# Kernel tuning notes

Measured on AMD Instinct MI355X. Metric: run time of the kernel, lower is better.

Reference implementation:

```python
import jax, jax.numpy as jnp
import numpy as np

N, G, H = 262144, 512, 16
EPS = 1e-5

Q_MAT = jnp.array([[0.0, 0.0, 1.0], [1.0, 0.0, 0.0], [0.0, 1.0, 0.0]], dtype=jnp.float32)
Q_TENSOR = jnp.kron(Q_MAT, Q_MAT)  # 9x9


def setup_inputs() -> dict:
    key = jax.random.key(0)
    ks = jax.random.split(key, 10)
    # sorted node->graph ids, every graph guaranteed non-empty
    gid = jnp.sort(jnp.concatenate([
        jnp.arange(G, dtype=jnp.int32),
        jax.random.randint(ks[0], (N - G,), 0, G, dtype=jnp.int32)]))
    return {
        'x00': jax.random.normal(ks[1], (N, 4 * H), jnp.float32),
        'x10': jax.random.normal(ks[2], (N, H, 3), jnp.float32),
        'x01': jax.random.normal(ks[3], (N, H, 3), jnp.float32),
        'x11': jax.random.normal(ks[4], (N, H, 9), jnp.float32),
        'pos': jax.random.normal(ks[5], (N, 6), jnp.float32),
        'graph_ids': gid,
        'num_graphs': G,
        'bn_gamma': jnp.ones((4 * H,), jnp.float32),
        'bn_beta': jnp.zeros((4 * H,), jnp.float32),
        'lin_w': jax.random.normal(ks[6], (3, 4 * H), jnp.float32) * 0.1,
        'lin_b': jnp.zeros((3,), jnp.float32),
        'w10': jax.random.normal(ks[7], (1, H), jnp.float32) * 0.3,
        'w01': jax.random.normal(ks[8], (1, H), jnp.float32) * 0.3,
        'w11': jax.random.normal(ks[9], (1, H), jnp.float32) * 0.3,
    }


def _graph_norm(x, seg, num_seg, gamma, beta):
    # per-graph mean/var normalization over nodes ('gn')
    cnt = jax.ops.segment_sum(jnp.ones((x.shape[0],), x.dtype), seg, num_segments=num_seg)
    cnt = jnp.maximum(cnt, 1.0)[:, None]
    mean = jax.ops.segment_sum(x, seg, num_segments=num_seg) / cnt
    var = jax.ops.segment_sum(x * x, seg, num_segments=num_seg) / cnt - mean * mean
    xn = (x - mean[seg]) * jax.lax.rsqrt(var[seg] + EPS)
    return xn * gamma + beta


def _segment_softmax(logits, seg, num_seg):
    m = jax.ops.segment_max(logits, seg, num_segments=num_seg)
    e = jnp.exp(logits - m[seg])
    s = jax.ops.segment_sum(e, seg, num_segments=num_seg)
    return e / s[seg]


def _project_r(r_vector):
    # SVD projection to nearest rotation (sign-corrected)
    norm = jnp.clip(jnp.linalg.norm(r_vector, axis=1, keepdims=True), 1e-5, None)
    r_vector = r_vector / jax.lax.stop_gradient(norm)  # norm is detached in torch
    # einops 'b (d c) -> b c d' with c=3
    r_ = jnp.transpose(r_vector.reshape(-1, 3, 3), (0, 2, 1))
    U, S, Vh = jnp.linalg.svd(r_, full_matrices=False)
    rot_pos = U @ Vh
    Vh_neg = Vh.at[:, 2, :].multiply(-1.0)
    rot_neg = U @ Vh_neg
    det = jnp.linalg.det(rot_pos)
    return jnp.where(det[:, None, None] > 0, rot_pos, rot_neg)


def reference(x00, x10, x01, x11, pos, graph_ids, num_graphs,
              bn_gamma, bn_beta, lin_w, lin_b, w10, w01, w11):
    seg = graph_ids
    Gn = num_graphs
    # BN('gn') + Linear -> 3 per-node logits
    xn = _graph_norm(x00, seg, Gn, bn_gamma, bn_beta)
    logits = xn @ lin_w.T + lin_b                       # [N,3]
    W = _segment_softmax(logits, seg, Gn)                # per-graph softmax over nodes
    w0, w1, w2 = W[:, 0:1], W[:, 1:2], W[:, 2:3]
    # weighted per-graph sums (dgl.sum_nodes)
    ab = jnp.concatenate([x10, x01], axis=-1)            # [N,H,6]
    mean_ab = jax.ops.segment_sum(ab * w1[:, :, None], seg, num_segments=Gn)   # [G,H,6]
    r_sum = jax.ops.segment_sum(x11 * w0[:, :, None], seg, num_segments=Gn)    # [G,H,9]
    m1m2 = jax.ops.segment_sum(pos * w2, seg, num_segments=Gn)                 # [G,6]
    m1, m2 = m1m2[:, 0:3], m1m2[:, 3:]
    # GLinear head: channel-mixing H -> 1 per degree type (no bias)
    out10 = jnp.einsum('oc,gcd->god', w10, mean_ab[:, :, :3])[:, 0, :]  # [G,3]
    out01 = jnp.einsum('oc,gcd->god', w01, mean_ab[:, :, 3:6])[:, 0, :]
    out11 = jnp.einsum('oc,gcd->god', w11, r_sum)[:, 0, :]              # [G,9]
    # permutation back to input frame
    r_vector = jnp.einsum('ij,gj->gi', Q_TENSOR, out11)
    trans_b = jnp.einsum('ij,gj->gi', Q_MAT, out01)
    trans_a = jnp.einsum('ij,gj->gi', Q_MAT, out10)
    rot_mat = _project_r(r_vector)
    t = m2 + trans_b - (rot_mat @ m1[..., None])[..., 0] - (rot_mat @ trans_a[..., None])[..., 0]
    return rot_mat, t, r_vector
```

## Files before the change

kernel.cpp:

```cpp
#include <hip/hip_runtime.h>
#include <cstdint>
#include <cstddef>

#define GG 512
#define NF 64
#define EPSF 1e-5f

__device__ __forceinline__ void atomAddF(float* p, float v) {
    unsafeAtomicAdd(p, v);
}

__global__ __launch_bounds__(256) void k_stats(const float* __restrict__ x00, const int* __restrict__ gid,
                        float* __restrict__ gsum, float* __restrict__ gsq,
                        float* __restrict__ gcnt, int N)
{
    int w = (blockIdx.x * blockDim.x + threadIdx.x) >> 6;
    int lane = threadIdx.x & 63;
    long base = (long)w * 64;
    int gf = gid[base];
    int gl = gid[base + 63];
    if (gf == gl) {
        const float4* p = reinterpret_cast<const float4*>(x00 + base * NF) + lane;
        float s0=0,s1=0,s2=0,s3=0,q0=0,q1=0,q2=0,q3=0;
        #pragma unroll
        for (int k = 0; k < 16; ++k) {
            float4 v = p[k * 64];
            s0+=v.x; s1+=v.y; s2+=v.z; s3+=v.w;
            q0=fmaf(v.x,v.x,q0); q1=fmaf(v.y,v.y,q1); q2=fmaf(v.z,v.z,q2); q3=fmaf(v.w,v.w,q3);
        }
        #pragma unroll
        for (int m = 16; m < 64; m <<= 1) {
            s0+=__shfl_xor(s0,m); s1+=__shfl_xor(s1,m); s2+=__shfl_xor(s2,m); s3+=__shfl_xor(s3,m);
            q0+=__shfl_xor(q0,m); q1+=__shfl_xor(q1,m); q2+=__shfl_xor(q2,m); q3+=__shfl_xor(q3,m);
        }
        if (lane < 16) {
            float* ds = gsum + gf * NF + lane * 4;
            float* dq = gsq  + gf * NF + lane * 4;
            atomAddF(ds+0,s0); atomAddF(ds+1,s1); atomAddF(ds+2,s2); atomAddF(ds+3,s3);
            atomAddF(dq+0,q0); atomAddF(dq+1,q1); atomAddF(dq+2,q2); atomAddF(dq+3,q3);
        }
        if (lane == 0) atomAddF(&gcnt[gf], 64.0f);
    } else {
        int myg = gid[base + lane];
        int cur = gf;
        float s = 0.f, q = 0.f, cnt = 0.f;
        for (int k = 0; k < 64; ++k) {
            int g = __shfl(myg, k);
            if (g != cur) {
                atomAddF(&gsum[cur * NF + lane], s);
                atomAddF(&gsq [cur * NF + lane], q);
                if (lane == 0) atomAddF(&gcnt[cur], cnt);
                s = q = cnt = 0.f; cur = g;
            }
            float v = x00[(base + k) * NF + lane];
            s += v; q = fmaf(v, v, q); cnt += 1.f;
        }
        atomAddF(&gsum[cur * NF + lane], s);
        atomAddF(&gsq [cur * NF + lane], q);
        if (lane == 0) atomAddF(&gcnt[cur], cnt);
    }
}

__global__ void k_prep(const float* __restrict__ gsum, const float* __restrict__ gsq,
                       const float* __restrict__ gcnt,
                       const float* __restrict__ gamma, const float* __restrict__ beta,
                       const float* __restrict__ lin_w, const float* __restrict__ lin_b,
                       float* __restrict__ Aeff, float* __restrict__ Beff)
{
    int g = blockIdx.x;
    int c = threadIdx.x;
    float cnt = fmaxf(gcnt[g], 1.f);
    float mean = gsum[g * NF + c] / cnt;
    float var  = gsq [g * NF + c] / cnt - mean * mean;
    float rs = rsqrtf(var + EPSF);
    float ga = gamma[c], be = beta[c];
    #pragma unroll
    for (int j = 0; j < 3; ++j) {
        float wv = lin_w[j * NF + c];
        Aeff[((long)g * 3 + j) * NF + c] = rs * ga * wv;
        float term = (be - mean * rs * ga) * wv;
        #pragma unroll
        for (int m = 32; m; m >>= 1) term += __shfl_xor(term, m);
        if (c == 0) Beff[g * 3 + j] = term + lin_b[j];
    }
}

__global__ __launch_bounds__(128) void k_logits(const float* __restrict__ x00, const int* __restrict__ gid,
                         const float* __restrict__ pos,
                         const float* __restrict__ Aeff, const float* __restrict__ Beff,
                         float* __restrict__ ebp, float* __restrict__ accum, int N)
{
    __shared__ float T2[2][64 * 68];
    int wid = threadIdx.x >> 6;
    int lane = threadIdx.x & 63;
    long chunk = (long)blockIdx.x * 2 + wid;
    long base = chunk * 64;
    float* T = T2[wid];

    const float* src = x00 + base * NF;
    #pragma unroll
    for (int k = 0; k < 16; ++k) {
        int fl = k * 256 + lane * 4;
        float4 v = *reinterpret_cast<const float4*>(src + fl);
        int n = fl >> 6, c = fl & 63;
        *reinterpret_cast<float4*>(&T[n * 68 + c]) = v;
    }
    __syncthreads();

    int gf = gid[base], gl = gid[base + 63];
    float l0, l1, l2;
    int g_l;
    if (gf == gl) {
        g_l = gf;
        const float* ap = Aeff + (size_t)gf * 192;
        float a0a=0,a0b=0,a1a=0,a1b=0,a2a=0,a2b=0;
        #pragma unroll
        for (int t = 0; t < 16; ++t) {
            float4 xv = *reinterpret_cast<const float4*>(&T[lane * 68 + 4 * t]);
            float4 w0 = *reinterpret_cast<const float4*>(ap + 4 * t);
            float4 w1 = *reinterpret_cast<const float4*>(ap + 64 + 4 * t);
            float4 w2 = *reinterpret_cast<const float4*>(ap + 128 + 4 * t);
            a0a = fmaf(xv.x,w0.x,fmaf(xv.y,w0.y,a0a)); a0b = fmaf(xv.z,w0.z,fmaf(xv.w,w0.w,a0b));
            a1a = fmaf(xv.x,w1.x,fmaf(xv.y,w1.y,a1a)); a1b = fmaf(xv.z,w1.z,fmaf(xv.w,w1.w,a1b));
            a2a = fmaf(xv.x,w2.x,fmaf(xv.y,w2.y,a2a)); a2b = fmaf(xv.z,w2.z,fmaf(xv.w,w2.w,a2b));
        }
        l0 = a0a + a0b + Beff[gf*3+0];
        l1 = a1a + a1b + Beff[gf*3+1];
        l2 = a2a + a2b + Beff[gf*3+2];
    } else {
        g_l = gid[base + lane];
        const float* ap = Aeff + (size_t)g_l * 192;
        float a0=0,a1=0,a2=0;
        #pragma unroll
        for (int t = 0; t < 16; ++t) {
            float4 xv = *reinterpret_cast<const float4*>(&T[lane * 68 + 4 * t]);
            float4 w0 = *reinterpret_cast<const float4*>(ap + 4 * t);
            float4 w1 = *reinterpret_cast<const float4*>(ap + 64 + 4 * t);
            float4 w2 = *reinterpret_cast<const float4*>(ap + 128 + 4 * t);
            a0 = fmaf(xv.x,w0.x,fmaf(xv.y,w0.y,fmaf(xv.z,w0.z,fmaf(xv.w,w0.w,a0))));
            a1 = fmaf(xv.x,w1.x,fmaf(xv.y,w1.y,fmaf(xv.z,w1.z,fmaf(xv.w,w1.w,a1))));
            a2 = fmaf(xv.x,w2.x,fmaf(xv.y,w2.y,fmaf(xv.z,w2.z,fmaf(xv.w,w2.w,a2))));
        }
        l0 = a0 + Beff[g_l*3+0];
        l1 = a1 + Beff[g_l*3+1];
        l2 = a2 + Beff[g_l*3+2];
    }
    float e0 = expf(l0), e1 = expf(l1), e2 = expf(l2);
    long node = base + lane;
    ebp[node]            = e0;
    ebp[(long)N + node]  = e1;
    ebp[2L * N + node]   = e2;

    const float* pp = pos + node * 6;
    float2 v01 = *reinterpret_cast<const float2*>(pp);
    float2 v23 = *reinterpret_cast<const float2*>(pp + 2);
    float2 v45 = *reinterpret_cast<const float2*>(pp + 4);
    float p0 = v01.x*e2, p1 = v01.y*e2, p2 = v23.x*e2, p3 = v23.y*e2, p4 = v45.x*e2, p5 = v45.y*e2;
    if (gf == gl) {
        #pragma unroll
        for (int m = 1; m < 64; m <<= 1) {
            e0+=__shfl_xor(e0,m); e1+=__shfl_xor(e1,m); e2+=__shfl_xor(e2,m);
            p0+=__shfl_xor(p0,m); p1+=__shfl_xor(p1,m); p2+=__shfl_xor(p2,m);
            p3+=__shfl_xor(p3,m); p4+=__shfl_xor(p4,m); p5+=__shfl_xor(p5,m);
        }
        if (lane == 0) {
            float* dst = accum + (long)gf * 32;
            atomAddF(dst+16,p0); atomAddF(dst+17,p1); atomAddF(dst+18,p2);
            atomAddF(dst+19,p3); atomAddF(dst+20,p4); atomAddF(dst+21,p5);
            atomAddF(dst+22,e0); atomAddF(dst+23,e1); atomAddF(dst+24,e2);
        }
    } else {
        float* dst = accum + (long)g_l * 32;
        atomAddF(dst+16,p0); atomAddF(dst+17,p1); atomAddF(dst+18,p2);
        atomAddF(dst+19,p3); atomAddF(dst+20,p4); atomAddF(dst+21,p5);
        atomAddF(dst+22,e0); atomAddF(dst+23,e1); atomAddF(dst+24,e2);
    }
}

__global__ __launch_bounds__(256) void k_wsum(const float* __restrict__ x10, const float* __restrict__ x01,
                       const float* __restrict__ x11,
                       const float* __restrict__ ebp, const int* __restrict__ gid,
                       const float* __restrict__ w10, const float* __restrict__ w01,
                       const float* __restrict__ w11,
                       float* __restrict__ accum, int N)
{
    __shared__ float Tb[4][240];
    int wid = threadIdx.x >> 6;
    int w = (blockIdx.x * blockDim.x + threadIdx.x) >> 6;
    int lane = threadIdx.x & 63;
    long base = (long)w * 64;
    float* T = Tb[wid];

    const float* p; long stride; const float* eb; int accOff; bool wr = true;
    float wt0, wt1, wt2, wt3;
    if (lane < 12) {
        p = x10 + lane * 4; stride = 48; eb = ebp + N; accOff = lane * 4;
        int f = lane * 4;
        wt0 = w10[f/3]; wt1 = w10[(f+1)/3]; wt2 = w10[(f+2)/3]; wt3 = w10[(f+3)/3];
    } else if (lane < 24) {
        p = x01 + (lane - 12) * 4; stride = 48; eb = ebp + N; accOff = 48 + (lane - 12) * 4;
        int f = (lane - 12) * 4;
        wt0 = w01[f/3]; wt1 = w01[(f+1)/3]; wt2 = w01[(f+2)/3]; wt3 = w01[(f+3)/3];
    } else if (lane < 60) {
        p = x11 + (lane - 24) * 4; stride = 144; eb = ebp; accOff = 96 + (lane - 24) * 4;
        int f = (lane - 24) * 4;
        wt0 = w11[f/9]; wt1 = w11[(f+1)/9]; wt2 = w11[(f+2)/9]; wt3 = w11[(f+3)/9];
    } else {
        p = x11 + 140; stride = 144; eb = ebp; accOff = 0; wr = false;
        wt0 = wt1 = wt2 = wt3 = 0.f;
    }

    float a0=0,a1=0,a2=0,a3=0;
    const float* pp = p + base * stride;
    const float* ep = eb + base;

    auto flush = [&](int g) {
        asm volatile("" ::: "memory");
        if (wr) {
            T[accOff+0] = a0*wt0; T[accOff+1] = a1*wt1;
            T[accOff+2] = a2*wt2; T[accOff+3] = a3*wt3;
        }
        asm volatile("s_waitcnt lgkmcnt(0)" ::: "memory");
        if (lane < 15) {
            int off, strd;
            if (lane < 3)      { off = lane;            strd = 3; }
            else if (lane < 6) { off = 48 + (lane - 3); strd = 3; }
            else               { off = 96 + (lane - 6); strd = 9; }
            float s = 0.f;
            #pragma unroll
            for (int c = 0; c < 16; ++c) s += T[off + c * strd];
            atomAddF(accum + (long)g * 32 + lane, s);
        }
        asm volatile("s_waitcnt lgkmcnt(0)" ::: "memory");
    };

    int gf = gid[base], gl = gid[base + 63];
    if (gf == gl) {
        #pragma unroll 8
        for (int k = 0; k < 64; ++k) {
            float e = ep[k];
            float4 v = *reinterpret_cast<const float4*>(pp + (long)k * stride);
            a0 = fmaf(v.x,e,a0); a1 = fmaf(v.y,e,a1); a2 = fmaf(v.z,e,a2); a3 = fmaf(v.w,e,a3);
        }
        flush(gf);
    } else {
        int myg = gid[base + lane];
        int cur = gf;
        for (int k = 0; k < 64; ++k) {
            int g = __shfl(myg, k);
            if (g != cur) { flush(cur); a0=a1=a2=a3=0.f; cur = g; }
            float e = ep[k];
            float4 v = *reinterpret_cast<const float4*>(pp + (long)k * stride);
            a0 = fmaf(v.x,e,a0); a1 = fmaf(v.y,e,a1); a2 = fmaf(v.z,e,a2); a3 = fmaf(v.w,e,a3);
        }
        flush(cur);
    }
}

#define JROT(p, q) do { \
    float apq_ = S[p][q]; \
    if (fabsf(apq_) > 1e-20f) { \
        float app_ = S[p][p], aqq_ = S[q][q]; \
        float tau_ = (aqq_ - app_) / (2.0f * apq_); \
        float tt_ = copysignf(1.0f, tau_) / (fabsf(tau_) + sqrtf(1.0f + tau_ * tau_)); \
        float cc_ = 1.0f / sqrtf(1.0f + tt_ * tt_); \
        float ssn_ = tt_ * cc_; \
        _Pragma("unroll") for (int kk = 0; kk < 3; ++kk) { \
            float skp = S[kk][p], skq = S[kk][q]; \
            S[kk][p] = cc_ * skp - ssn_ * skq; S[kk][q] = ssn_ * skp + cc_ * skq; } \
        _Pragma("unroll") for (int kk = 0; kk < 3; ++kk) { \
            float spk = S[p][kk], sqk = S[q][kk]; \
            S[p][kk] = cc_ * spk - ssn_ * sqk; S[q][kk] = ssn_ * spk + cc_ * sqk; } \
        _Pragma("unroll") for (int kk = 0; kk < 3; ++kk) { \
            float vkp = V[kk][p], vkq = V[kk][q]; \
            V[kk][p] = cc_ * vkp - ssn_ * vkq; V[kk][q] = ssn_ * vkp + cc_ * vkq; } \
    } \
} while (0)

__global__ void k_final(const float* __restrict__ accum, float* __restrict__ out)
{
    int g = blockIdx.x * blockDim.x + threadIdx.x;
    if (g >= GG) return;
    const float* A_ = accum + (long)g * 32;
    float i0 = 1.f / A_[22], i1 = 1.f / A_[23], i2 = 1.f / A_[24];

    float o10[3], o01[3], o11[9];
    #pragma unroll
    for (int d = 0; d < 3; ++d) { o10[d] = A_[d] * i1; o01[d] = A_[3 + d] * i1; }
    #pragma unroll
    for (int d = 0; d < 9; ++d) o11[d] = A_[6 + d] * i0;

    float m1v[3], m2v[3];
    #pragma unroll
    for (int d = 0; d < 3; ++d) { m1v[d] = A_[16 + d] * i2; m2v[d] = A_[19 + d] * i2; }

    int sig[3]; sig[0] = 2; sig[1] = 0; sig[2] = 1;
    float rv[9];
    #pragma unroll
    for (int a = 0; a < 3; ++a)
        #pragma unroll
        for (int b = 0; b < 3; ++b)
            rv[a * 3 + b] = o11[sig[a] * 3 + sig[b]];
    float ta[3], tb[3];
    #pragma unroll
    for (int a = 0; a < 3; ++a) { ta[a] = o10[sig[a]]; tb[a] = o01[sig[a]]; }

    float nn = 0.f;
    #pragma unroll
// ... 56 lines not shown
    R[0][2] = u0x * e0z + u1x * e1z + u2x * c2z;
    R[1][0] = u0y * e0x + u1y * e1x + u2y * c2x;
    R[1][1] = u0y * e0y + u1y * e1y + u2y * c2y;
    R[1][2] = u0y * e0z + u1y * e1z + u2y * c2z;
    R[2][0] = u0z * e0x + u1z * e1x + u2z * c2x;
    R[2][1] = u0z * e0y + u1z * e1y + u2z * c2y;
    R[2][2] = u0z * e0z + u1z * e1z + u2z * c2z;

    float tv[3];
    #pragma unroll
    for (int a = 0; a < 3; ++a) {
        float acc = m2v[a] + tb[a];
        #pragma unroll
        for (int b = 0; b < 3; ++b) acc -= R[a][b] * (m1v[b] + ta[b]);
        tv[a] = acc;
    }

    #pragma unroll
    for (int k = 0; k < 9; ++k) out[(long)g * 9 + k] = R[k / 3][k % 3];
    #pragma unroll
    for (int a = 0; a < 3; ++a) out[(long)GG * 9 + (long)g * 3 + a] = tv[a];
    #pragma unroll
    for (int k = 0; k < 9; ++k) out[(long)GG * 12 + (long)g * 9 + k] = rv[k];
}

extern "C" void kernel_launch(void* const* d_in, const int* in_sizes, int n_in,
                              void* d_out, int out_size, void* d_ws, size_t ws_size,
                              hipStream_t stream)
{
    const float* x00   = (const float*)d_in[0];
    const float* x10   = (const float*)d_in[1];
    const float* x01   = (const float*)d_in[2];
    const float* x11   = (const float*)d_in[3];
    const float* pos   = (const float*)d_in[4];
    const int*   gid   = (const int*)d_in[5];
    const float* gamma = (const float*)d_in[7];
    const float* beta  = (const float*)d_in[8];
    const float* lin_w = (const float*)d_in[9];
    const float* lin_b = (const float*)d_in[10];
    const float* w10   = (const float*)d_in[11];
    const float* w01   = (const float*)d_in[12];
    const float* w11   = (const float*)d_in[13];
    float* out = (float*)d_out;

    const int N = in_sizes[0] / NF;

    float* ws = (float*)d_ws;
    float* gsum  = ws;
    float* gsq   = gsum + GG * 64;
    float* gcnt  = gsq + GG * 64;
    float* accum = gcnt + GG;
    float* Aeff  = accum + GG * 32;
    float* Beff  = Aeff + GG * 192;
    float* ebp   = Beff + GG * 3;

    size_t zeroBytes = (size_t)(GG * 64 * 2 + GG + GG * 32) * sizeof(float);
    hipMemsetAsync(d_ws, 0, zeroBytes, stream);

    int nwave64 = N / 64;
    int blocks64 = nwave64 / 4;
    int blocksLg = (N / 64) / 2;

    k_stats <<<blocks64, 256, 0, stream>>>(x00, gid, gsum, gsq, gcnt, N);
    k_prep  <<<GG, 64, 0, stream>>>(gsum, gsq, gcnt, gamma, beta, lin_w, lin_b, Aeff, Beff);
    k_logits<<<blocksLg, 128, 0, stream>>>(x00, gid, pos, Aeff, Beff, ebp, accum, N);
    k_wsum  <<<blocks64, 256, 0, stream>>>(x10, x01, x11, ebp, gid, w10, w01, w11, accum, N);
    k_final <<<(GG + 63) / 64, 64, 0, stream>>>(accum, out);
}
```

Before: 187.5 us.

## Split weighted-sum kernel into LDS-staged x11 and x10/x01 kernels

Replaces the single wave-per-64-nodes weighted-sum kernel, which had strided per-lane float4 loads, with two block-per-64-nodes kernels. Each block loads its tile coalesced into shared memory and applies the H-channel mixing per node before the segment reduction. Uniform-graph tiles are reduced through shared memory with one atomic per output. Mixed tiles instead issue per-element atomics, which adds an extra kernel launch and more shared-memory traffic and occupancy pressure (about 37KB LDS per block for x11).

```diff
diff --git a/kernel.cpp b/kernel.cpp
--- a/kernel.cpp
+++ b/kernel.cpp
@@ -177,83 +177,142 @@
     }
 }
 
-__global__ __launch_bounds__(256) void k_wsum(const float* __restrict__ x10, const float* __restrict__ x01,
-                       const float* __restrict__ x11,
-                       const float* __restrict__ ebp, const int* __restrict__ gid,
-                       const float* __restrict__ w10, const float* __restrict__ w01,
-                       const float* __restrict__ w11,
-                       float* __restrict__ accum, int N)
-{
-    __shared__ float Tb[4][240];
-    int wid = threadIdx.x >> 6;
-    int w = (blockIdx.x * blockDim.x + threadIdx.x) >> 6;
-    int lane = threadIdx.x & 63;
-    long base = (long)w * 64;
-    float* T = Tb[wid];
-
-    const float* p; long stride; const float* eb; int accOff; bool wr = true;
-    float wt0, wt1, wt2, wt3;
-    if (lane < 12) {
-        p = x10 + lane * 4; stride = 48; eb = ebp + N; accOff = lane * 4;
-        int f = lane * 4;
-        wt0 = w10[f/3]; wt1 = w10[(f+1)/3]; wt2 = w10[(f+2)/3]; wt3 = w10[(f+3)/3];
-    } else if (lane < 24) {
-        p = x01 + (lane - 12) * 4; stride = 48; eb = ebp + N; accOff = 48 + (lane - 12) * 4;
-        int f = (lane - 12) * 4;
-        wt0 = w01[f/3]; wt1 = w01[(f+1)/3]; wt2 = w01[(f+2)/3]; wt3 = w01[(f+3)/3];
-    } else if (lane < 60) {
-        p = x11 + (lane - 24) * 4; stride = 144; eb = ebp; accOff = 96 + (lane - 24) * 4;
-        int f = (lane - 24) * 4;
-        wt0 = w11[f/9]; wt1 = w11[(f+1)/9]; wt2 = w11[(f+2)/9]; wt3 = w11[(f+3)/9];
-    } else {
-        p = x11 + 140; stride = 144; eb = ebp; accOff = 0; wr = false;
-        wt0 = wt1 = wt2 = wt3 = 0.f;
-    }
-
-    float a0=0,a1=0,a2=0,a3=0;
-    const float* pp = p + base * stride;
-    const float* ep = eb + base;
-
-    auto flush = [&](int g) {
-        asm volatile("" ::: "memory");
-        if (wr) {
-            T[accOff+0] = a0*wt0; T[accOff+1] = a1*wt1;
-            T[accOff+2] = a2*wt2; T[accOff+3] = a3*wt3;
-        }
-        asm volatile("s_waitcnt lgkmcnt(0)" ::: "memory");
-        if (lane < 15) {
-            int off, strd;
-            if (lane < 3)      { off = lane;            strd = 3; }
-            else if (lane < 6) { off = 48 + (lane - 3); strd = 3; }
-            else               { off = 96 + (lane - 6); strd = 9; }
+__global__ __launch_bounds__(256) void k_w11(const float* __restrict__ x11,
+        const float* __restrict__ ebp, const int* __restrict__ gid,
+        const float* __restrict__ w11, float* __restrict__ accum, int N)
+{
+    __shared__ float LD[64 * 148];
+    __shared__ float EE[64];
+    int tid = threadIdx.x;
+    long tb = (long)blockIdx.x * 64;
+
+    const float4* src = reinterpret_cast<const float4*>(x11 + tb * 144);
+    float4 v[9];
+    #pragma unroll
+    for (int u = 0; u < 9; ++u) v[u] = src[tid + 256 * u];
+    if (tid < 64) EE[tid] = ebp[tb + tid];
+
+    #pragma unroll
+    for (int u = 0; u < 9; ++u) {
+        int fi = 4 * (tid + 256 * u);
+        int n = fi / 144, k = fi % 144;
+        *reinterpret_cast<float4*>(&LD[n * 148 + k]) = v[u];
+    }
+    __syncthreads();
+
+    float w[16];
+    #pragma unroll
+    for (int c = 0; c < 16; ++c) w[c] = w11[c];
+
+    float y[3]; int nn[3], dd[3];
+    #pragma unroll
+    for (int r = 0; r < 3; ++r) {
+        int idx = tid + 256 * r;
+        nn[r] = idx / 9; dd[r] = idx - 9 * nn[r];
+        y[r] = 0.f;
+        if (r < 2 || tid < 64) {
             float s = 0.f;
             #pragma unroll
-            for (int c = 0; c < 16; ++c) s += T[off + c * strd];
-            atomAddF(accum + (long)g * 32 + lane, s);
-        }
-        asm volatile("s_waitcnt lgkmcnt(0)" ::: "memory");
-    };
-
-    int gf = gid[base], gl = gid[base + 63];
+            for (int c = 0; c < 16; ++c)
+                s = fmaf(w[c], LD[nn[r] * 148 + c * 9 + dd[r]], s);
+            y[r] = EE[nn[r]] * s;
+        }
+    }
+
+    int gf = gid[tb], gl = gid[tb + 63];
     if (gf == gl) {
-        #pragma unroll 8
-        for (int k = 0; k < 64; ++k) {
-            float e = ep[k];
-            float4 v = *reinterpret_cast<const float4*>(pp + (long)k * stride);
-            a0 = fmaf(v.x,e,a0); a1 = fmaf(v.y,e,a1); a2 = fmaf(v.z,e,a2); a3 = fmaf(v.w,e,a3);
-        }
-        flush(gf);
+        __syncthreads();
+        float* F = LD;
+        #pragma unroll
+        for (int r = 0; r < 3; ++r)
+            if (r < 2 || tid < 64) F[dd[r] * 64 + nn[r]] = y[r];
+        __syncthreads();
+        if (tid < 9) {
+            float s = 0.f;
+            #pragma unroll
+            for (int n = 0; n < 64; ++n) s += F[tid * 64 + n];
+            atomAddF(accum + (long)gf * 32 + 6 + tid, s);
+        }
     } else {
-        int myg = gid[base + lane];
-        int cur = gf;
-        for (int k = 0; k < 64; ++k) {
-            int g = __shfl(myg, k);
-            if (g != cur) { flush(cur); a0=a1=a2=a3=0.f; cur = g; }
-            float e = ep[k];
-            float4 v = *reinterpret_cast<const float4*>(pp + (long)k * stride);
-            a0 = fmaf(v.x,e,a0); a1 = fmaf(v.y,e,a1); a2 = fmaf(v.z,e,a2); a3 = fmaf(v.w,e,a3);
-        }
-        flush(cur);
+        #pragma unroll
+        for (int r = 0; r < 3; ++r)
+            if (r < 2 || tid < 64)
+                atomAddF(accum + (long)gid[tb + nn[r]] * 32 + 6 + dd[r], y[r]);
+    }
+}
+
+__global__ __launch_bounds__(256) void k_w1001(const float* __restrict__ x10,
+        const float* __restrict__ x01, const float* __restrict__ ebp,
+        const int* __restrict__ gid,
+        const float* __restrict__ w10, const float* __restrict__ w01,
+        float* __restrict__ accum, int N)
+{
+    __shared__ float LDa[64 * 52];
+    __shared__ float LDb[64 * 52];
+    __shared__ float EE[64];
+    int tid = threadIdx.x;
+    long tb = (long)blockIdx.x * 64;
+
+    const float4* sa = reinterpret_cast<const float4*>(x10 + tb * 48);
+    const float4* sb = reinterpret_cast<const float4*>(x01 + tb * 48);
+    float4 va[3], vb[3];
+    #pragma unroll
+    for (int u = 0; u < 3; ++u) { va[u] = sa[tid + 256 * u]; vb[u] = sb[tid + 256 * u]; }
+    if (tid < 64) EE[tid] = ebp[(long)N + tb + tid];
+
+    #pragma unroll
+    for (int u = 0; u < 3; ++u) {
+        int fi = 4 * (tid + 256 * u);
+        int n = fi / 48, k = fi % 48;
+        *reinterpret_cast<float4*>(&LDa[n * 52 + k]) = va[u];
+        *reinterpret_cast<float4*>(&LDb[n * 52 + k]) = vb[u];
+    }
+    __syncthreads();
+
+    float wA[16], wB[16];
+    #pragma unroll
+    for (int c = 0; c < 16; ++c) { wA[c] = w10[c]; wB[c] = w01[c]; }
+
+    float y[2]; int nn[2], dd[2], ar[2];
+    #pragma unroll
+    for (int r = 0; r < 2; ++r) {
+        int idx = tid + 256 * r;
+        ar[r] = idx / 192;
+        int j = idx - 192 * ar[r];
+        nn[r] = j / 3; dd[r] = j - 3 * nn[r];
+        y[r] = 0.f;
+        if (r < 1 || tid < 128) {
+            const float* Lx = ar[r] ? LDb : LDa;
+            float s = 0.f;
+            #pragma unroll
+            for (int c = 0; c < 16; ++c) {
+                float wc = ar[r] ? wB[c] : wA[c];
+                s = fmaf(wc, Lx[nn[r] * 52 + c * 3 + dd[r]], s);
+            }
+            y[r] = EE[nn[r]] * s;
+        }
+    }
+
+    int gf = gid[tb], gl = gid[tb + 63];
+    if (gf == gl) {
+        __syncthreads();
+        float* F = LDa;
+        #pragma unroll
+        for (int r = 0; r < 2; ++r)
+            if (r < 1 || tid < 128) F[ar[r] * 192 + dd[r] * 64 + nn[r]] = y[r];
+        __syncthreads();
+        if (tid < 6) {
+            int a = tid / 3, d = tid - 3 * a;
+            float s = 0.f;
+            #pragma unroll
+            for (int n = 0; n < 64; ++n) s += F[a * 192 + d * 64 + n];
+            atomAddF(accum + (long)gf * 32 + a * 3 + d, s);
+        }
+    } else {
+        #pragma unroll
+        for (int r = 0; r < 2; ++r)
+            if (r < 1 || tid < 128)
+                atomAddF(accum + (long)gid[tb + nn[r]] * 32 + ar[r] * 3 + dd[r], y[r]);
     }
 }
 
@@ -421,13 +480,14 @@
     size_t zeroBytes = (size_t)(GG * 64 * 2 + GG + GG * 32) * sizeof(float);
     hipMemsetAsync(d_ws, 0, zeroBytes, stream);
 
-    int nwave64 = N / 64;
-    int blocks64 = nwave64 / 4;
-    int blocksLg = (N / 64) / 2;
-
-    k_stats <<<blocks64, 256, 0, stream>>>(x00, gid, gsum, gsq, gcnt, N);
+    int blocksA = (N / 64) / 4;
+    int blocksL = (N / 64) / 2;
+    int blocksT = N / 64;
+
+    k_stats <<<blocksA, 256, 0, stream>>>(x00, gid, gsum, gsq, gcnt, N);
     k_prep  <<<GG, 64, 0, stream>>>(gsum, gsq, gcnt, gamma, beta, lin_w, lin_b, Aeff, Beff);
-    k_logits<<<blocksLg, 128, 0, stream>>>(x00, gid, pos, Aeff, Beff, ebp, accum, N);
-    k_wsum  <<<blocks64, 256, 0, stream>>>(x10, x01, x11, ebp, gid, w10, w01, w11, accum, N);
+    k_logits<<<blocksL, 128, 0, stream>>>(x00, gid, pos, Aeff, Beff, ebp, accum, N);
+    k_w11   <<<blocksT, 256, 0, stream>>>(x11, ebp, gid, w11, accum, N);
+    k_w1001 <<<blocksT, 256, 0, stream>>>(x10, x01, ebp, gid, w10, w01, accum, N);
     k_final <<<(GG + 63) / 64, 64, 0, stream>>>(accum, out);
 }
```

Result: faster. 180.0 us (-4.0%).

## Contract channel weights per node early and fold weighted sums into logits pass

Applied to the files above, without the earlier changes.

Applies the H->1 channel mixing for x10, x01 and x11 per node inside a merged stats kernel, writing a compact 16-float-per-node buffer. The logits kernel then multiplies these by the softmax exponentials and reduces them alongside the existing sums, removing the separate weighted-sum kernel and the exponential buffer. This aims to cut a launch and replace the strided wsum reduction with a simple per-node contraction running concurrently with the statistics pass, at the cost of an extra 16 MB intermediate and more shuffles and atomics in the logits kernel. Block partitioning is hardcoded to the fixed problem size.

```diff
diff --git a/kernel.cpp b/kernel.cpp
--- a/kernel.cpp
+++ b/kernel.cpp
@@ -10,54 +10,137 @@
     unsafeAtomicAdd(p, v);
 }
 
-__global__ __launch_bounds__(256) void k_stats(const float* __restrict__ x00, const int* __restrict__ gid,
-                        float* __restrict__ gsum, float* __restrict__ gsq,
-                        float* __restrict__ gcnt, int N)
+__global__ __launch_bounds__(256) void k_mega(const float* __restrict__ x00,
+        const float* __restrict__ x10, const float* __restrict__ x01,
+        const float* __restrict__ x11, const int* __restrict__ gid,
+        const float* __restrict__ w10, const float* __restrict__ w01,
+        const float* __restrict__ w11,
+        float* __restrict__ gsum, float* __restrict__ gsq,
+        float* __restrict__ gcnt, float* __restrict__ y, int N)
 {
-    int w = (blockIdx.x * blockDim.x + threadIdx.x) >> 6;
-    int lane = threadIdx.x & 63;
-    long base = (long)w * 64;
-    int gf = gid[base];
-    int gl = gid[base + 63];
-    if (gf == gl) {
-        const float4* p = reinterpret_cast<const float4*>(x00 + base * NF) + lane;
-        float s0=0,s1=0,s2=0,s3=0,q0=0,q1=0,q2=0,q3=0;
-        #pragma unroll
-        for (int k = 0; k < 16; ++k) {
-            float4 v = p[k * 64];
-            s0+=v.x; s1+=v.y; s2+=v.z; s3+=v.w;
-            q0=fmaf(v.x,v.x,q0); q1=fmaf(v.y,v.y,q1); q2=fmaf(v.z,v.z,q2); q3=fmaf(v.w,v.w,q3);
-        }
-        #pragma unroll
-        for (int m = 16; m < 64; m <<= 1) {
-            s0+=__shfl_xor(s0,m); s1+=__shfl_xor(s1,m); s2+=__shfl_xor(s2,m); s3+=__shfl_xor(s3,m);
-            q0+=__shfl_xor(q0,m); q1+=__shfl_xor(q1,m); q2+=__shfl_xor(q2,m); q3+=__shfl_xor(q3,m);
-        }
-        if (lane < 16) {
-            float* ds = gsum + gf * NF + lane * 4;
-            float* dq = gsq  + gf * NF + lane * 4;
-            atomAddF(ds+0,s0); atomAddF(ds+1,s1); atomAddF(ds+2,s2); atomAddF(ds+3,s3);
-            atomAddF(dq+0,q0); atomAddF(dq+1,q1); atomAddF(dq+2,q2); atomAddF(dq+3,q3);
-        }
-        if (lane == 0) atomAddF(&gcnt[gf], 64.0f);
+    const int bid = blockIdx.x;
+    const int tid = threadIdx.x;
+
+    if (bid < 1024) {
+        int w = (bid * 256 + tid) >> 6;
+        int lane = tid & 63;
+        long base = (long)w * 64;
+        int gf = gid[base];
+        int gl = gid[base + 63];
+        if (gf == gl) {
+            const float4* p = reinterpret_cast<const float4*>(x00 + base * NF) + lane;
+            float s0=0,s1=0,s2=0,s3=0,q0=0,q1=0,q2=0,q3=0;
+            #pragma unroll
+            for (int k = 0; k < 16; ++k) {
+                float4 v = p[k * 64];
+                s0+=v.x; s1+=v.y; s2+=v.z; s3+=v.w;
+                q0=fmaf(v.x,v.x,q0); q1=fmaf(v.y,v.y,q1); q2=fmaf(v.z,v.z,q2); q3=fmaf(v.w,v.w,q3);
+            }
+            #pragma unroll
+            for (int m = 16; m < 64; m <<= 1) {
+                s0+=__shfl_xor(s0,m); s1+=__shfl_xor(s1,m); s2+=__shfl_xor(s2,m); s3+=__shfl_xor(s3,m);
+                q0+=__shfl_xor(q0,m); q1+=__shfl_xor(q1,m); q2+=__shfl_xor(q2,m); q3+=__shfl_xor(q3,m);
+            }
+            if (lane < 16) {
+                float* ds = gsum + gf * NF + lane * 4;
+                float* dq = gsq  + gf * NF + lane * 4;
+                atomAddF(ds+0,s0); atomAddF(ds+1,s1); atomAddF(ds+2,s2); atomAddF(ds+3,s3);
+                atomAddF(dq+0,q0); atomAddF(dq+1,q1); atomAddF(dq+2,q2); atomAddF(dq+3,q3);
+            }
+            if (lane == 0) atomAddF(&gcnt[gf], 64.0f);
+        } else {
+            int myg = gid[base + lane];
+            int cur = gf;
+            float s = 0.f, q = 0.f, cnt = 0.f;
+            for (int k = 0; k < 64; ++k) {
+                int g = __shfl(myg, k);
+                if (g != cur) {
+                    atomAddF(&gsum[cur * NF + lane], s);
+                    atomAddF(&gsq [cur * NF + lane], q);
+                    if (lane == 0) atomAddF(&gcnt[cur], cnt);
+                    s = q = cnt = 0.f; cur = g;
+                }
+                float v = x00[(base + k) * NF + lane];
+                s += v; q = fmaf(v, v, q); cnt += 1.f;
+            }
+            atomAddF(&gsum[cur * NF + lane], s);
+            atomAddF(&gsq [cur * NF + lane], q);
+            if (lane == 0) atomAddF(&gcnt[cur], cnt);
+        }
+    } else if (bid < 2048) {
+        const long nb = (long)(bid - 1024) * 256;
+        const int q = tid & 3;
+        float wq[4];
+        #pragma unroll
+        for (int c = 0; c < 4; ++c) wq[c] = w11[4 * q + c];
+
+        for (int r = 0; r < 4; ++r) {
+            long row = nb + r * 64 + (tid >> 2);
+            const float4* s = reinterpret_cast<const float4*>(x11 + row * 144) + q * 9;
+            float4 B[9];
+            #pragma unroll
+            for (int j = 0; j < 9; ++j) B[j] = s[j];
+            float z[9] = {0,0,0,0,0,0,0,0,0};
+            #pragma unroll
+            for (int j = 0; j < 9; ++j) {
+                const int i0 = 4 * j;
+                z[(i0 + 0) % 9] = fmaf(wq[(i0 + 0) / 9], B[j].x, z[(i0 + 0) % 9]);
+                z[(i0 + 1) % 9] = fmaf(wq[(i0 + 1) / 9], B[j].y, z[(i0 + 1) % 9]);
+                z[(i0 + 2) % 9] = fmaf(wq[(i0 + 2) / 9], B[j].z, z[(i0 + 2) % 9]);
+                z[(i0 + 3) % 9] = fmaf(wq[(i0 + 3) / 9], B[j].w, z[(i0 + 3) % 9]);
+            }
+            #pragma unroll
+            for (int d = 0; d < 9; ++d) {
+                z[d] += __shfl_xor(z[d], 1);
+                z[d] += __shfl_xor(z[d], 2);
+            }
+            float* yr = y + row * 16;
+            yr[q]     = (q == 0) ? z[0] : (q == 1) ? z[1] : (q == 2) ? z[2] : z[3];
+            yr[4 + q] = (q == 0) ? z[4] : (q == 1) ? z[5] : (q == 2) ? z[6] : z[7];
+            if (q == 0) yr[8] = z[8];
+        }
     } else {
-        int myg = gid[base + lane];
-        int cur = gf;
-        float s = 0.f, q = 0.f, cnt = 0.f;
-        for (int k = 0; k < 64; ++k) {
-            int g = __shfl(myg, k);
-            if (g != cur) {
-                atomAddF(&gsum[cur * NF + lane], s);
-                atomAddF(&gsq [cur * NF + lane], q);
-                if (lane == 0) atomAddF(&gcnt[cur], cnt);
-                s = q = cnt = 0.f; cur = g;
-            }
-            float v = x00[(base + k) * NF + lane];
-            s += v; q = fmaf(v, v, q); cnt += 1.f;
-        }
-        atomAddF(&gsum[cur * NF + lane], s);
-        atomAddF(&gsq [cur * NF + lane], q);
-        if (lane == 0) atomAddF(&gcnt[cur], cnt);
+        const long row = (long)(bid - 2048) * 256 + tid;
+        {
+            float wA[16];
+            #pragma unroll
+            for (int c = 0; c < 16; ++c) wA[c] = w10[c];
+            const float4* s = reinterpret_cast<const float4*>(x10 + row * 48);
+            float4 B[12];
+            #pragma unroll
+            for (int j = 0; j < 12; ++j) B[j] = s[j];
+            float z[3] = {0, 0, 0};
+            #pragma unroll
+            for (int j = 0; j < 12; ++j) {
+                const int i0 = 4 * j;
+                z[(i0 + 0) % 3] = fmaf(wA[(i0 + 0) / 3], B[j].x, z[(i0 + 0) % 3]);
+                z[(i0 + 1) % 3] = fmaf(wA[(i0 + 1) / 3], B[j].y, z[(i0 + 1) % 3]);
+                z[(i0 + 2) % 3] = fmaf(wA[(i0 + 2) / 3], B[j].z, z[(i0 + 2) % 3]);
+                z[(i0 + 3) % 3] = fmaf(wA[(i0 + 3) / 3], B[j].w, z[(i0 + 3) % 3]);
+            }
+            float* yr = y + row * 16 + 9;
+            yr[0] = z[0]; yr[1] = z[1]; yr[2] = z[2];
+        }
+        {
+            float wB[16];
+            #pragma unroll
+            for (int c = 0; c < 16; ++c) wB[c] = w01[c];
+            const float4* s = reinterpret_cast<const float4*>(x01 + row * 48);
+            float4 B[12];
+            #pragma unroll
+            for (int j = 0; j < 12; ++j) B[j] = s[j];
+            float z[3] = {0, 0, 0};
+            #pragma unroll
+            for (int j = 0; j < 12; ++j) {
+                const int i0 = 4 * j;
+                z[(i0 + 0) % 3] = fmaf(wB[(i0 + 0) / 3], B[j].x, z[(i0 + 0) % 3]);
+                z[(i0 + 1) % 3] = fmaf(wB[(i0 + 1) / 3], B[j].y, z[(i0 + 1) % 3]);
+                z[(i0 + 2) % 3] = fmaf(wB[(i0 + 2) / 3], B[j].z, z[(i0 + 2) % 3]);
+                z[(i0 + 3) % 3] = fmaf(wB[(i0 + 3) / 3], B[j].w, z[(i0 + 3) % 3]);
+            }
+            float* yr = y + row * 16 + 12;
+            yr[0] = z[0]; yr[1] = z[1]; yr[2] = z[2];
+        }
     }
 }
 
@@ -86,9 +169,9 @@
 }
 
 __global__ __launch_bounds__(128) void k_logits(const float* __restrict__ x00, const int* __restrict__ gid,
-                         const float* __restrict__ pos,
+                         const float* __restrict__ pos, const float* __restrict__ yv,
                          const float* __restrict__ Aeff, const float* __restrict__ Beff,
-                         float* __restrict__ ebp, float* __restrict__ accum, int N)
+                         float* __restrict__ accum, int N)
 {
     __shared__ float T2[2][64 * 68];
     int wid = threadIdx.x >> 6;
@@ -147,113 +230,56 @@
     }
     float e0 = expf(l0), e1 = expf(l1), e2 = expf(l2);
     long node = base + lane;
-    ebp[node]            = e0;
-    ebp[(long)N + node]  = e1;
-    ebp[2L * N + node]   = e2;
+
+    const float4* yp = reinterpret_cast<const float4*>(yv + node * 16);
+    float4 y0 = yp[0], y1 = yp[1], y2 = yp[2], y3 = yp[3];
+    float va[9], vb[3], vc[3];
+    va[0]=e0*y0.x; va[1]=e0*y0.y; va[2]=e0*y0.z; va[3]=e0*y0.w;
+    va[4]=e0*y1.x; va[5]=e0*y1.y; va[6]=e0*y1.z; va[7]=e0*y1.w;
+    va[8]=e0*y2.x;
+    vb[0]=e1*y2.y; vb[1]=e1*y2.z; vb[2]=e1*y2.w;
+    vc[0]=e1*y3.x; vc[1]=e1*y3.y; vc[2]=e1*y3.z;
 
     const float* pp = pos + node * 6;
     float2 v01 = *reinterpret_cast<const float2*>(pp);
     float2 v23 = *reinterpret_cast<const float2*>(pp + 2);
     float2 v45 = *reinterpret_cast<const float2*>(pp + 4);
     float p0 = v01.x*e2, p1 = v01.y*e2, p2 = v23.x*e2, p3 = v23.y*e2, p4 = v45.x*e2, p5 = v45.y*e2;
+
     if (gf == gl) {
         #pragma unroll
         for (int m = 1; m < 64; m <<= 1) {
+            #pragma unroll
+            for (int d = 0; d < 9; ++d) va[d] += __shfl_xor(va[d], m);
+            #pragma unroll
+            for (int d = 0; d < 3; ++d) { vb[d]+=__shfl_xor(vb[d],m); vc[d]+=__shfl_xor(vc[d],m); }
             e0+=__shfl_xor(e0,m); e1+=__shfl_xor(e1,m); e2+=__shfl_xor(e2,m);
             p0+=__shfl_xor(p0,m); p1+=__shfl_xor(p1,m); p2+=__shfl_xor(p2,m);
             p3+=__shfl_xor(p3,m); p4+=__shfl_xor(p4,m); p5+=__shfl_xor(p5,m);
         }
         if (lane == 0) {
             float* dst = accum + (long)gf * 32;
+            #pragma unroll
+            for (int d = 0; d < 3; ++d) atomAddF(dst + d, vb[d]);
+            #pragma unroll
+            for (int d = 0; d < 3; ++d) atomAddF(dst + 3 + d, vc[d]);
+            #pragma unroll
+            for (int d = 0; d < 9; ++d) atomAddF(dst + 6 + d, va[d]);
             atomAddF(dst+16,p0); atomAddF(dst+17,p1); atomAddF(dst+18,p2);
             atomAddF(dst+19,p3); atomAddF(dst+20,p4); atomAddF(dst+21,p5);
             atomAddF(dst+22,e0); atomAddF(dst+23,e1); atomAddF(dst+24,e2);
         }
     } else {
         float* dst = accum + (long)g_l * 32;
+        #pragma unroll
+        for (int d = 0; d < 3; ++d) atomAddF(dst + d, vb[d]);
+        #pragma unroll
+        for (int d = 0; d < 3; ++d) atomAddF(dst + 3 + d, vc[d]);
+        #pragma unroll
+        for (int d = 0; d < 9; ++d) atomAddF(dst + 6 + d, va[d]);
         atomAddF(dst+16,p0); atomAddF(dst+17,p1); atomAddF(dst+18,p2);
         atomAddF(dst+19,p3); atomAddF(dst+20,p4); atomAddF(dst+21,p5);
         atomAddF(dst+22,e0); atomAddF(dst+23,e1); atomAddF(dst+24,e2);
-    }
-}
-
-__global__ __launch_bounds__(256) void k_wsum(const float* __restrict__ x10, const float* __restrict__ x01,
-                       const float* __restrict__ x11,
-                       const float* __restrict__ ebp, const int* __restrict__ gid,
-                       const float* __restrict__ w10, const float* __restrict__ w01,
-                       const float* __restrict__ w11,
-                       float* __restrict__ accum, int N)
-{
-    __shared__ float Tb[4][240];
-    int wid = threadIdx.x >> 6;
-    int w = (blockIdx.x * blockDim.x + threadIdx.x) >> 6;
-    int lane = threadIdx.x & 63;
-    long base = (long)w * 64;
-    float* T = Tb[wid];
-
-    const float* p; long stride; const float* eb; int accOff; bool wr = true;
-    float wt0, wt1, wt2, wt3;
-    if (lane < 12) {
-        p = x10 + lane * 4; stride = 48; eb = ebp + N; accOff = lane * 4;
-        int f = lane * 4;
-        wt0 = w10[f/3]; wt1 = w10[(f+1)/3]; wt2 = w10[(f+2)/3]; wt3 = w10[(f+3)/3];
-    } else if (lane < 24) {
-        p = x01 + (lane - 12) * 4; stride = 48; eb = ebp + N; accOff = 48 + (lane - 12) * 4;
-        int f = (lane - 12) * 4;
-        wt0 = w01[f/3]; wt1 = w01[(f+1)/3]; wt2 = w01[(f+2)/3]; wt3 = w01[(f+3)/3];
-    } else if (lane < 60) {
-        p = x11 + (lane - 24) * 4; stride = 144; eb = ebp; accOff = 96 + (lane - 24) * 4;
-        int f = (lane - 24) * 4;
-        wt0 = w11[f/9]; wt1 = w11[(f+1)/9]; wt2 = w11[(f+2)/9]; wt3 = w11[(f+3)/9];
-    } else {
-        p = x11 + 140; stride = 144; eb = ebp; accOff = 0; wr = false;
-        wt0 = wt1 = wt2 = wt3 = 0.f;
-    }
-
-    float a0=0,a1=0,a2=0,a3=0;
-    const float* pp = p + base * stride;
-    const float* ep = eb + base;
-
-    auto flush = [&](int g) {
-        asm volatile("" ::: "memory");
-        if (wr) {
-            T[accOff+0] = a0*wt0; T[accOff+1] = a1*wt1;
-            T[accOff+2] = a2*wt2; T[accOff+3] = a3*wt3;
-        }
-        asm volatile("s_waitcnt lgkmcnt(0)" ::: "memory");
-        if (lane < 15) {
-            int off, strd;
-            if (lane < 3)      { off = lane;            strd = 3; }
-            else if (lane < 6) { off = 48 + (lane - 3); strd = 3; }
-            else               { off = 96 + (lane - 6); strd = 9; }
-            float s = 0.f;
-            #pragma unroll
-            for (int c = 0; c < 16; ++c) s += T[off + c * strd];
-            atomAddF(accum + (long)g * 32 + lane, s);
-        }
-        asm volatile("s_waitcnt lgkmcnt(0)" ::: "memory");
-    };
-
-    int gf = gid[base], gl = gid[base + 63];
-    if (gf == gl) {
-        #pragma unroll 8
-        for (int k = 0; k < 64; ++k) {
-            float e = ep[k];
-            float4 v = *reinterpret_cast<const float4*>(pp + (long)k * stride);
-            a0 = fmaf(v.x,e,a0); a1 = fmaf(v.y,e,a1); a2 = fmaf(v.z,e,a2); a3 = fmaf(v.w,e,a3);
-        }
-        flush(gf);
-    } else {
-        int myg = gid[base + lane];
-        int cur = gf;
-        for (int k = 0; k < 64; ++k) {
-            int g = __shfl(myg, k);
-            if (g != cur) { flush(cur); a0=a1=a2=a3=0.f; cur = g; }
-            float e = ep[k];
-            float4 v = *reinterpret_cast<const float4*>(pp + (long)k * stride);
-            a0 = fmaf(v.x,e,a0); a1 = fmaf(v.y,e,a1); a2 = fmaf(v.z,e,a2); a3 = fmaf(v.w,e,a3);
-        }
-        flush(cur);
     }
 }
 
@@ -416,18 +442,17 @@
     float* accum = gcnt + GG;
     float* Aeff  = accum + GG * 32;
     float* Beff  = Aeff + GG * 192;
-    float* ebp   = Beff + GG * 3;
+    float* yv    = Beff + GG * 3;
 
     size_t zeroBytes = (size_t)(GG * 64 * 2 + GG + GG * 32) * sizeof(float);
     hipMemsetAsync(d_ws, 0, zeroBytes, stream);
 
-    int nwave64 = N / 64;
-    int blocks64 = nwave64 / 4;
-    int blocksLg = (N / 64) / 2;
-
-    k_stats <<<blocks64, 256, 0, stream>>>(x00, gid, gsum, gsq, gcnt, N);
+    int blocksM = 3072;
+    int blocksL = (N / 64) / 2;
+
+    k_mega  <<<blocksM, 256, 0, stream>>>(x00, x10, x01, x11, gid, w10, w01, w11,
+                                          gsum, gsq, gcnt, yv, N);
     k_prep  <<<GG, 64, 0, stream>>>(gsum, gsq, gcnt, gamma, beta, lin_w, lin_b, Aeff, Beff);
-    k_logits<<<blocksLg, 128, 0, stream>>>(x00, gid, pos, Aeff, Beff, ebp, accum, N);
-    k_wsum  <<<blocks64, 256, 0, stream>>>(x10, x01, x11, ebp, gid, w10, w01, w11, accum, N);
+    k_logits<<<blocksL, 128, 0, stream>>>(x00, gid, pos, yv, Aeff, Beff, accum, N);
     k_final <<<(GG + 63) / 64, 64, 0, stream>>>(accum, out);
 }
```

Measured after the change: 248.9 us. +32.7%, slower.

## Restructure weighted-sum kernel for coalesced contiguous loads with split x11/xab blocks

Applied to the files above, without the earlier changes.

The weighted-sum kernel is rewritten so each wave reads 16-node chunks of x11 (or x10/x01) as fully contiguous float4 runs, rather than the old per-lane strided loads where lanes 60-63 sat idle. Per-node softmax weights are broadcast with shuffles, and partial sums are kept in rotated register slots that are reduced through LDS at graph boundaries. Chunks that span two graphs fall back to per-element atomics. Even and odd blocks now handle the x11 and x10/x01 streams separately, and the unused third ebp write in the logits kernel is dropped. The cost is higher register pressure and possible heavy atomic traffic in boundary chunks.

```diff
diff --git a/kernel.cpp b/kernel.cpp
--- a/kernel.cpp
+++ b/kernel.cpp
@@ -149,7 +149,6 @@
     long node = base + lane;
     ebp[node]            = e0;
     ebp[(long)N + node]  = e1;
-    ebp[2L * N + node]   = e2;
 
     const float* pp = pos + node * 6;
     float2 v01 = *reinterpret_cast<const float2*>(pp);
@@ -177,83 +176,203 @@
     }
 }
 
-__global__ __launch_bounds__(256) void k_wsum(const float* __restrict__ x10, const float* __restrict__ x01,
-                       const float* __restrict__ x11,
-                       const float* __restrict__ ebp, const int* __restrict__ gid,
-                       const float* __restrict__ w10, const float* __restrict__ w01,
-                       const float* __restrict__ w11,
-                       float* __restrict__ accum, int N)
+__global__ __launch_bounds__(256, 4) void k_wsum(const float* __restrict__ x10,
+        const float* __restrict__ x01, const float* __restrict__ x11,
+        const float* __restrict__ ebp, const int* __restrict__ gid,
+        const float* __restrict__ w10, const float* __restrict__ w01,
+        const float* __restrict__ w11, float* __restrict__ accum, int N)
 {
-    __shared__ float Tb[4][240];
-    int wid = threadIdx.x >> 6;
-    int w = (blockIdx.x * blockDim.x + threadIdx.x) >> 6;
-    int lane = threadIdx.x & 63;
-    long base = (long)w * 64;
-    float* T = Tb[wid];
-
-    const float* p; long stride; const float* eb; int accOff; bool wr = true;
-    float wt0, wt1, wt2, wt3;
-    if (lane < 12) {
-        p = x10 + lane * 4; stride = 48; eb = ebp + N; accOff = lane * 4;
-        int f = lane * 4;
-        wt0 = w10[f/3]; wt1 = w10[(f+1)/3]; wt2 = w10[(f+2)/3]; wt3 = w10[(f+3)/3];
-    } else if (lane < 24) {
-        p = x01 + (lane - 12) * 4; stride = 48; eb = ebp + N; accOff = 48 + (lane - 12) * 4;
-        int f = (lane - 12) * 4;
-        wt0 = w01[f/3]; wt1 = w01[(f+1)/3]; wt2 = w01[(f+2)/3]; wt3 = w01[(f+3)/3];
-    } else if (lane < 60) {
-        p = x11 + (lane - 24) * 4; stride = 144; eb = ebp; accOff = 96 + (lane - 24) * 4;
-        int f = (lane - 24) * 4;
-        wt0 = w11[f/9]; wt1 = w11[(f+1)/9]; wt2 = w11[(f+2)/9]; wt3 = w11[(f+3)/9];
+    __shared__ float LDSW[4][576];
+    const int tid = threadIdx.x;
+    const int wid = tid >> 6;
+    const int lane = tid & 63;
+    float* L = LDSW[wid];
+
+    if ((blockIdx.x & 1) == 0) {
+        const long base = ((long)(blockIdx.x >> 1) * 4 + wid) * 64;
+        const float e_regf = ebp[base + lane];
+        const int   g_reg  = gid[base + lane];
+
+        int nj[9]; float wvx[9], wvy[9], wvz[9], wvw[9];
+        #pragma unroll
+        for (int j = 0; j < 9; ++j) {
+            int f0 = 4 * (lane + 64 * j);
+            nj[j] = (f0 % 2304) / 144;
+            int rem = f0 % 144;
+            wvx[j] = w11[(rem + 0) / 9];
+            wvy[j] = w11[(rem + 1) / 9];
+            wvz[j] = w11[(rem + 2) / 9];
+            wvw[j] = w11[(rem + 3) / 9];
+        }
+        const int r = (4 * lane) % 9;
+        int rot[9];
+        #pragma unroll
+        for (int s = 0; s < 9; ++s) rot[s] = (r + s) % 9;
+
+        float z[9];
+        #pragma unroll
+        for (int s = 0; s < 9; ++s) z[s] = 0.f;
+        int cur = __shfl(g_reg, 0);
+        bool dirty = false;
+
+        auto flushZ = [&](int g) {
+            if (!dirty) return;
+            #pragma unroll
+            for (int s = 0; s < 9; ++s) L[lane * 9 + rot[s]] = z[s];
+            asm volatile("s_waitcnt lgkmcnt(0)" ::: "memory");
+            __builtin_amdgcn_sched_barrier(0);
+            if (lane < 9) {
+                float sum = 0.f;
+                for (int m = 0; m < 64; ++m) sum += L[m * 9 + lane];
+                atomAddF(accum + (long)g * 32 + 6 + lane, sum);
+            }
+            asm volatile("s_waitcnt lgkmcnt(0) vmcnt(0)" ::: "memory");
+            #pragma unroll
+            for (int s = 0; s < 9; ++s) z[s] = 0.f;
+            dirty = false;
+        };
+
+        #define X11ACC(J) do { \
+            const float en = __shfl(e_regf, t16 + nj[J]); \
+            z[(4*(J)+0)%9] = fmaf(en * wvx[J], B##J.x, z[(4*(J)+0)%9]); \
+            z[(4*(J)+1)%9] = fmaf(en * wvy[J], B##J.y, z[(4*(J)+1)%9]); \
+            z[(4*(J)+2)%9] = fmaf(en * wvz[J], B##J.z, z[(4*(J)+2)%9]); \
+            z[(4*(J)+3)%9] = fmaf(en * wvw[J], B##J.w, z[(4*(J)+3)%9]); \
+        } while (0)
+
+        #define X11ATOM(J) do { \
+            const int nn = t16 + nj[J]; \
+            const float en = __shfl(e_regf, nn); \
+            const int   gg = __shfl(g_reg,  nn); \
+            float* dst = accum + (long)gg * 32 + 6; \
+            atomAddF(dst + rot[(4*(J)+0)%9], en * wvx[J] * B##J.x); \
+            atomAddF(dst + rot[(4*(J)+1)%9], en * wvy[J] * B##J.y); \
+            atomAddF(dst + rot[(4*(J)+2)%9], en * wvz[J] * B##J.z); \
+            atomAddF(dst + rot[(4*(J)+3)%9], en * wvw[J] * B##J.w); \
+        } while (0)
+
+        for (int t = 0; t < 4; ++t) {
+            const int t16 = t * 16;
+            const float4* s4 = reinterpret_cast<const float4*>(x11 + (base + t16) * 144);
+            float4 B0 = s4[lane];
+            float4 B1 = s4[lane + 64];
+            float4 B2 = s4[lane + 128];
+            float4 B3 = s4[lane + 192];
+            float4 B4 = s4[lane + 256];
+            float4 B5 = s4[lane + 320];
+            float4 B6 = s4[lane + 384];
+            float4 B7 = s4[lane + 448];
+            float4 B8 = s4[lane + 512];
+            int gft = __shfl(g_reg, t16), glt = __shfl(g_reg, t16 + 15);
+            if (gft == glt) {
+                if (gft != cur) { flushZ(cur); cur = gft; }
+                X11ACC(0); X11ACC(1); X11ACC(2); X11ACC(3); X11ACC(4);
+                X11ACC(5); X11ACC(6); X11ACC(7); X11ACC(8);
+                dirty = true;
+            } else {
+                flushZ(cur);
+                X11ATOM(0); X11ATOM(1); X11ATOM(2); X11ATOM(3); X11ATOM(4);
+                X11ATOM(5); X11ATOM(6); X11ATOM(7); X11ATOM(8);
+                cur = glt;
+            }
+        }
+        flushZ(cur);
     } else {
-        p = x11 + 140; stride = 144; eb = ebp; accOff = 0; wr = false;
-        wt0 = wt1 = wt2 = wt3 = 0.f;
-    }
-
-    float a0=0,a1=0,a2=0,a3=0;
-    const float* pp = p + base * stride;
-    const float* ep = eb + base;
-
-    auto flush = [&](int g) {
-        asm volatile("" ::: "memory");
-        if (wr) {
-            T[accOff+0] = a0*wt0; T[accOff+1] = a1*wt1;
-            T[accOff+2] = a2*wt2; T[accOff+3] = a3*wt3;
-        }
-        asm volatile("s_waitcnt lgkmcnt(0)" ::: "memory");
-        if (lane < 15) {
-            int off, strd;
-            if (lane < 3)      { off = lane;            strd = 3; }
-            else if (lane < 6) { off = 48 + (lane - 3); strd = 3; }
-            else               { off = 96 + (lane - 6); strd = 9; }
-            float s = 0.f;
+        const long base = ((long)(blockIdx.x >> 1) * 4 + wid) * 64;
+        const float e_regf = ebp[(long)N + base + lane];
+        const int   g_reg  = gid[base + lane];
+
+        int nj[3]; float axx[3], axy[3], axz[3], axw[3], bxx[3], bxy[3], bxz[3], bxw[3];
+        #pragma unroll
+        for (int j = 0; j < 3; ++j) {
+            int f0 = 4 * (lane + 64 * j);
+            nj[j] = f0 / 48;
+            int rem = f0 % 48;
+            axx[j] = w10[(rem + 0) / 3]; axy[j] = w10[(rem + 1) / 3];
+            axz[j] = w10[(rem + 2) / 3]; axw[j] = w10[(rem + 3) / 3];
+            bxx[j] = w01[(rem + 0) / 3]; bxy[j] = w01[(rem + 1) / 3];
+            bxz[j] = w01[(rem + 2) / 3]; bxw[j] = w01[(rem + 3) / 3];
+        }
+        const int r3 = lane % 3;
+        int rot3[3];
+        #pragma unroll
+        for (int s = 0; s < 3; ++s) rot3[s] = (r3 + s) % 3;
+
+        float zA[3], zB[3];
+        #pragma unroll
+        for (int s = 0; s < 3; ++s) { zA[s] = 0.f; zB[s] = 0.f; }
+        int cur = __shfl(g_reg, 0);
+        bool dirty = false;
+
+        auto flushZ = [&](int g) {
+            if (!dirty) return;
             #pragma unroll
-            for (int c = 0; c < 16; ++c) s += T[off + c * strd];
-            atomAddF(accum + (long)g * 32 + lane, s);
-        }
-        asm volatile("s_waitcnt lgkmcnt(0)" ::: "memory");
-    };
-
-    int gf = gid[base], gl = gid[base + 63];
-    if (gf == gl) {
-        #pragma unroll 8
-        for (int k = 0; k < 64; ++k) {
-            float e = ep[k];
-            float4 v = *reinterpret_cast<const float4*>(pp + (long)k * stride);
-            a0 = fmaf(v.x,e,a0); a1 = fmaf(v.y,e,a1); a2 = fmaf(v.z,e,a2); a3 = fmaf(v.w,e,a3);
-        }
-        flush(gf);
-    } else {
-        int myg = gid[base + lane];
-        int cur = gf;
-        for (int k = 0; k < 64; ++k) {
-            int g = __shfl(myg, k);
-            if (g != cur) { flush(cur); a0=a1=a2=a3=0.f; cur = g; }
-            float e = ep[k];
-            float4 v = *reinterpret_cast<const float4*>(pp + (long)k * stride);
-            a0 = fmaf(v.x,e,a0); a1 = fmaf(v.y,e,a1); a2 = fmaf(v.z,e,a2); a3 = fmaf(v.w,e,a3);
-        }
-        flush(cur);
+            for (int s = 0; s < 3; ++s) {
+                L[lane * 6 + rot3[s]]     = zA[s];
+                L[lane * 6 + 3 + rot3[s]] = zB[s];
+            }
+            asm volatile("s_waitcnt lgkmcnt(0)" ::: "memory");
+            __builtin_amdgcn_sched_barrier(0);
+            if (lane < 6) {
+                float sum = 0.f;
+                for (int m = 0; m < 64; ++m) sum += L[m * 6 + lane];
+                atomAddF(accum + (long)g * 32 + lane, sum);
+            }
+            asm volatile("s_waitcnt lgkmcnt(0) vmcnt(0)" ::: "memory");
+            #pragma unroll
+            for (int s = 0; s < 3; ++s) { zA[s] = 0.f; zB[s] = 0.f; }
+            dirty = false;
+        };
+
+        #define XABACC(J) do { \
+            const float en = __shfl(e_regf, t16 + nj[J]); \
+            zA[((J)+0)%3] = fmaf(en * axx[J], A##J.x, zA[((J)+0)%3]); \
+            zA[((J)+1)%3] = fmaf(en * axy[J], A##J.y, zA[((J)+1)%3]); \
+            zA[((J)+2)%3] = fmaf(en * axz[J], A##J.z, zA[((J)+2)%3]); \
+            zA[((J)+3)%3] = fmaf(en * axw[J], A##J.w, zA[((J)+3)%3]); \
+            zB[((J)+0)%3] = fmaf(en * bxx[J], C##J.x, zB[((J)+0)%3]); \
+            zB[((J)+1)%3] = fmaf(en * bxy[J], C##J.y, zB[((J)+1)%3]); \
+            zB[((J)+2)%3] = fmaf(en * bxz[J], C##J.z, zB[((J)+2)%3]); \
+            zB[((J)+3)%3] = fmaf(en * bxw[J], C##J.w, zB[((J)+3)%3]); \
+        } while (0)
+
+        #define XABATOM(J) do { \
+            const int nn = t16 + nj[J]; \
+            const float en = __shfl(e_regf, nn); \
+            const int   gg = __shfl(g_reg,  nn); \
+            float* dst = accum + (long)gg * 32; \
+            atomAddF(dst + rot3[((J)+0)%3], en * axx[J] * A##J.x); \
+            atomAddF(dst + rot3[((J)+1)%3], en * axy[J] * A##J.y); \
+            atomAddF(dst + rot3[((J)+2)%3], en * axz[J] * A##J.z); \
+            atomAddF(dst + rot3[((J)+3)%3], en * axw[J] * A##J.w); \
+            atomAddF(dst + 3 + rot3[((J)+0)%3], en * bxx[J] * C##J.x); \
+            atomAddF(dst + 3 + rot3[((J)+1)%3], en * bxy[J] * C##J.y); \
+            atomAddF(dst + 3 + rot3[((J)+2)%3], en * bxz[J] * C##J.z); \
+            atomAddF(dst + 3 + rot3[((J)+3)%3], en * bxw[J] * C##J.w); \
+        } while (0)
+
+        for (int t = 0; t < 4; ++t) {
+            const int t16 = t * 16;
+            const float4* sa = reinterpret_cast<const float4*>(x10 + (base + t16) * 48);
+            const float4* sb = reinterpret_cast<const float4*>(x01 + (base + t16) * 48);
+            float4 A0 = sa[lane];
+            float4 A1 = sa[lane + 64];
+            float4 A2 = sa[lane + 128];
+            float4 C0 = sb[lane];
+            float4 C1 = sb[lane + 64];
+            float4 C2 = sb[lane + 128];
+            int gft = __shfl(g_reg, t16), glt = __shfl(g_reg, t16 + 15);
+            if (gft == glt) {
+                if (gft != cur) { flushZ(cur); cur = gft; }
+                XABACC(0); XABACC(1); XABACC(2);
+                dirty = true;
+            } else {
+                flushZ(cur);
+                XABATOM(0); XABATOM(1); XABATOM(2);
+                cur = glt;
+            }
+        }
+        flushZ(cur);
     }
 }
 
@@ -421,13 +540,13 @@
     size_t zeroBytes = (size_t)(GG * 64 * 2 + GG + GG * 32) * sizeof(float);
     hipMemsetAsync(d_ws, 0, zeroBytes, stream);
 
-    int nwave64 = N / 64;
-    int blocks64 = nwave64 / 4;
-    int blocksLg = (N / 64) / 2;
-
-    k_stats <<<blocks64, 256, 0, stream>>>(x00, gid, gsum, gsq, gcnt, N);
+    int blocksA = (N / 64) / 4;
+    int blocksL = (N / 64) / 2;
+    int blocksD = 2 * (N / 256);
+
+    k_stats <<<blocksA, 256, 0, stream>>>(x00, gid, gsum, gsq, gcnt, N);
     k_prep  <<<GG, 64, 0, stream>>>(gsum, gsq, gcnt, gamma, beta, lin_w, lin_b, Aeff, Beff);
-    k_logits<<<blocksLg, 128, 0, stream>>>(x00, gid, pos, Aeff, Beff, ebp, accum, N);
-    k_wsum  <<<blocks64, 256, 0, stream>>>(x10, x01, x11, ebp, gid, w10, w01, w11, accum, N);
+    k_logits<<<blocksL, 128, 0, stream>>>(x00, gid, pos, Aeff, Beff, ebp, accum, N);
+    k_wsum  <<<blocksD, 256, 0, stream>>>(x10, x01, x11, ebp, gid, w10, w01, w11, accum, N);
     k_final <<<(GG + 63) / 64, 64, 0, stream>>>(accum, out);
 }
```

New measurement: 247.1 us. 1.32x slower.
